# Optimization experiments

Hardware: AMD Instinct MI355X
Metric: run time of the kernel (lower is better)

The kernel has to match this reference:

```python
import jax, jax.numpy as jnp
import numpy as np

N = 100000
E = 3200000
F_IN = 128
H1 = 16
H2 = 8
NEG_SLOPE = 0.2


def _gat_layer(x, src, dst, W, a_src, a_dst, b, n_nodes):
    # x: [N, Fin]; src/dst: [E_tot] (self-loops included); W: [Fin, Fout]
    h = x @ W                                   # [N, Fout]
    e_src = h @ a_src                           # [N]
    e_dst = h @ a_dst                           # [N]
    e = e_src[src] + e_dst[dst]                 # [E_tot]
    e = jnp.where(e > 0, e, NEG_SLOPE * e)      # leaky_relu(0.2)
    m = jax.ops.segment_max(e, dst, num_segments=n_nodes)   # [N]
    w = jnp.exp(e - m[dst])                     # [E_tot]
    s = jax.ops.segment_sum(w, dst, num_segments=n_nodes)   # [N]
    alpha = w / s[dst]                          # [E_tot]
    out = jax.ops.segment_sum(alpha[:, None] * h[src], dst, num_segments=n_nodes)
    return out + b


def setup_inputs() -> dict:
    key = jax.random.key(0)
    ks = jax.random.split(key, 12)
    x = jax.random.normal(ks[0], (N, F_IN), dtype=jnp.float32)
    edge_index = jax.random.randint(ks[1], (E, 2), 0, N, dtype=jnp.int64)
    s1 = 1.0 / np.sqrt(F_IN)
    s2 = 1.0 / np.sqrt(H1)
    s3 = 1.0 / np.sqrt(H2)
    return {
        "x": x,
        "edge_index": edge_index,
        "W1": jax.random.normal(ks[2], (F_IN, H1), dtype=jnp.float32) * s1,
        "a1_src": jax.random.normal(ks[3], (H1,), dtype=jnp.float32) * s2,
        "a1_dst": jax.random.normal(ks[4], (H1,), dtype=jnp.float32) * s2,
        "b1": jnp.zeros((H1,), dtype=jnp.float32),
        "W2": jax.random.normal(ks[5], (H1, H2), dtype=jnp.float32) * s2,
        "a2_src": jax.random.normal(ks[6], (H2,), dtype=jnp.float32) * s3,
        "a2_dst": jax.random.normal(ks[7], (H2,), dtype=jnp.float32) * s3,
        "b2": jnp.zeros((H2,), dtype=jnp.float32),
        "Wf": jax.random.normal(ks[8], (H2, 1), dtype=jnp.float32) * s3,
        "bf": jnp.zeros((1,), dtype=jnp.float32),
    }


def reference(x, edge_index, W1, a1_src, a1_dst, b1, W2, a2_src, a2_dst, b2, Wf, bf):
    ei = edge_index.T                            # [2, E] as in original forward
    loop = jnp.arange(N, dtype=ei.dtype)
    src = jnp.concatenate([ei[0], loop])         # PyG add_self_loops=True
    dst = jnp.concatenate([ei[1], loop])
    h = jax.nn.relu(_gat_layer(x, src, dst, W1, a1_src, a1_dst, b1, N))
    # dropout p=0.05 is identity at inference
    h = jax.nn.relu(_gat_layer(h, src, dst, W2, a2_src, a2_dst, b2, N))
    return h @ Wf + bf                           # [N, 1]
```

## Files before the change

### kernel.cpp

```cpp
#include <hip/hip_runtime.h>
#include <math.h>

#define N_NODES 100000
#define N_EDGES 3200000
#define E_TOT   (N_EDGES + N_NODES)
#define F_IN    128
#define H1      16
#define H2      8
#define NEG     0.2f
#define NBUCKET ((N_NODES + 255) >> 8)
#define NCHUNK  512
#define CE      ((N_EDGES + NCHUNK - 1) / NCHUNK)

__global__ __launch_bounds__(256) void k1_xw(
        const float* __restrict__ x, const float* __restrict__ W1,
        const float* __restrict__ a1s, const float* __restrict__ a1d,
        float* __restrict__ h1, float* __restrict__ e1s, float* __restrict__ e1d) {
    __shared__ float w1s[F_IN * H1];
    __shared__ float xs[16 * 132];
    __shared__ float a1ss[H1], a1ds[H1];
    const int tid = threadIdx.x;
    for (int i = tid; i < F_IN * H1; i += 256) w1s[i] = W1[i];
    if (tid < H1) { a1ss[tid] = a1s[tid]; a1ds[tid] = a1d[tid]; }
    const int rowbase = blockIdx.x * 16;
    #pragma unroll
    for (int i = 0; i < 2; i++) {
        int q = tid + i * 256;
        int r = q >> 5, c = q & 31;
        float4 v = *(const float4*)(x + (size_t)(rowbase + r) * F_IN + c * 4);
        *(float4*)(xs + r * 132 + c * 4) = v;
    }
    __syncthreads();
    const int g = tid >> 4, j = tid & 15;
    const float* xrow = xs + g * 132;
    float acc = 0.f;
    #pragma unroll 8
    for (int k = 0; k < F_IN; k++) acc += xrow[k] * w1s[k * H1 + j];
    const int row = rowbase + g;
    h1[(size_t)row * H1 + j] = acc;
    float ps = acc * a1ss[j];
    float pd = acc * a1ds[j];
    #pragma unroll
    for (int m = 8; m >= 1; m >>= 1) {
        ps += __shfl_xor(ps, m, 16);
        pd += __shfl_xor(pd, m, 16);
    }
    if (j == 0) { e1s[row] = ps; e1d[row] = pd; }
}


__global__ __launch_bounds__(256) void k_count(const int2* __restrict__ ei,
                                               int* __restrict__ counts) {
    __shared__ int hist[NBUCKET];
    for (int i = threadIdx.x; i < NBUCKET; i += 256) hist[i] = 0;
    __syncthreads();
    const int b = blockIdx.x;
    const int beg = b * CE, end = min(N_EDGES, beg + CE);
    for (int e = beg + threadIdx.x; e < end; e += 256)
        atomicAdd(&hist[ei[e].y >> 8], 1);
    __syncthreads();
    for (int i = threadIdx.x; i < NBUCKET; i += 256)
        counts[i * NCHUNK + b] = hist[i];
}

__global__ __launch_bounds__(512) void k_scanA(int* __restrict__ counts,
                                               int* __restrict__ btot) {
    __shared__ int lds[NCHUNK];
    const int k = blockIdx.x, t = threadIdx.x;
    int v = counts[k * NCHUNK + t];
    lds[t] = v;
    __syncthreads();
    for (int off = 1; off < NCHUNK; off <<= 1) {
        int u = (t >= off) ? lds[t - off] : 0;
        __syncthreads();
        lds[t] += u;
        __syncthreads();
    }
    counts[k * NCHUNK + t] = lds[t] - v;
    if (t == NCHUNK - 1) btot[k] = lds[t];
}

__global__ __launch_bounds__(512) void k_scanB(const int* __restrict__ btot,
                                               int* __restrict__ bbase) {
    __shared__ int lds[512];
    const int t = threadIdx.x;
    int v = (t < NBUCKET) ? btot[t] : 0;
    lds[t] = v;
    __syncthreads();
    for (int off = 1; off < 512; off <<= 1) {
        int u = (t >= off) ? lds[t - off] : 0;
        __syncthreads();
        lds[t] += u;
        __syncthreads();
    }
    if (t < NBUCKET) bbase[t] = lds[t] - v;
    if (t == 511) bbase[NBUCKET] = lds[511];
}

__global__ __launch_bounds__(256) void k_reorder(const int2* __restrict__ ei,
                                                 const int* __restrict__ counts,
                                                 const int* __restrict__ bbase,
                                                 int* __restrict__ pairs) {
    __shared__ int cur[NBUCKET];
    const int b = blockIdx.x;
    for (int i = threadIdx.x; i < NBUCKET; i += 256)
        cur[i] = bbase[i] + counts[i * NCHUNK + b];
    __syncthreads();
    const int beg = b * CE, end = min(N_EDGES, beg + CE);
    for (int e = beg + threadIdx.x; e < end; e += 256) {
        int2 v = ei[e];
        int k = v.y >> 8;
        int pos = atomicAdd(&cur[k], 1);
        pairs[pos] = (v.x << 8) | (v.y & 255);
    }
}

__global__ __launch_bounds__(256) void k_csr(const int* __restrict__ pairs,
                                             const int* __restrict__ bbase,
                                             int* __restrict__ rowg,
                                             int* __restrict__ degg,
                                             int* __restrict__ sorted_src) {
    __shared__ int deg[256], scn[256], cur[256];
    const int k = blockIdx.x, t = threadIdx.x;
    const int n0 = k << 8;
    const int nn = min(256, N_NODES - n0);
    deg[t] = 0;
    __syncthreads();
    const int ebeg = bbase[k], eend = bbase[k + 1];
    for (int e = ebeg + t; e < eend; e += 256)
        atomicAdd(&deg[pairs[e] & 255], 1);
    __syncthreads();
    int v = (t < nn) ? deg[t] : 0;
    scn[t] = v;
    __syncthreads();
    for (int off = 1; off < 256; off <<= 1) {
        int u = (t >= off) ? scn[t - off] : 0;
        __syncthreads();
        scn[t] += u;
        __syncthreads();
    }
    int excl = scn[t] - v;
    if (t < nn) {
        int r = ebeg + excl + n0 + t;
        rowg[n0 + t] = r;
        degg[n0 + t] = v + 1;
        sorted_src[r] = n0 + t;
        cur[t] = r + 1;
    }
    __syncthreads();
    for (int e = ebeg + t; e < eend; e += 256) {
        int p = pairs[e];
        int pos = atomicAdd(&cur[p & 255], 1);
        sorted_src[pos] = p >> 8;
    }
}

template <int LPN, bool LAYER2>
__global__ __launch_bounds__(256) void k_agg(
        const int* __restrict__ row, const int* __restrict__ deg,
        const int* __restrict__ sorted_src,
        const float* __restrict__ es, const float* __restrict__ ed,
        const float* __restrict__ h, const float* __restrict__ b,
        const float* __restrict__ Wf, const float* __restrict__ bf,
        float* __restrict__ h_out, float* __restrict__ out) {
    const int sub = threadIdx.x & (LPN - 1);
    const int node = (blockIdx.x * 256 + threadIdx.x) / LPN;
    if (node >= N_NODES) return;
    const int beg = row[node];
    const int cnt = deg[node];
    const float edv = ed[node];
    const float4* h4 = (const float4*)h;
    float4 acc = make_float4(0.f, 0.f, 0.f, 0.f);
    float s = 0.f;
    int src_a = sorted_src[beg];
    int src_b = (cnt > 1) ? sorted_src[beg + 1] : src_a;
    float ev_a = es[src_a];
    float4 hv_a = h4[(size_t)src_a * LPN + sub];
    for (int t = 0; t < cnt; t++) {
        int src_c = (t + 2 < cnt) ? sorted_src[beg + t + 2] : src_b;
        float ev_b = es[src_b];
        float4 hv_b = h4[(size_t)src_b * LPN + sub];
        float e = ev_a + edv;
        e = e > 0.f ? e : NEG * e;
        float p = __expf(e);
        s += p;
        acc.x += p * hv_a.x;
        acc.y += p * hv_a.y;
        acc.z += p * hv_a.z;
        acc.w += p * hv_a.w;
        src_b = src_c; ev_a = ev_b; hv_a = hv_b;
    }
    const float inv = 1.f / s;
    const float4 b4 = ((const float4*)b)[sub];
    float4 o;
    o.x = fmaxf(acc.x * inv + b4.x, 0.f);
    o.y = fmaxf(acc.y * inv + b4.y, 0.f);
    o.z = fmaxf(acc.z * inv + b4.z, 0.f);
    o.w = fmaxf(acc.w * inv + b4.w, 0.f);
    if (!LAYER2) {
        ((float4*)h_out)[(size_t)node * LPN + sub] = o;
    } else {
        const float4 w4 = ((const float4*)Wf)[sub];
        float r = o.x * w4.x + o.y * w4.y + o.z * w4.z + o.w * w4.w;
        r += __shfl_xor(r, 1, 2);
        if (sub == 0) out[node] = r + bf[0];
    }
}

__global__ __launch_bounds__(256) void k_mid(
        const float* __restrict__ h1f, const float* __restrict__ W2,
        const float* __restrict__ a2s, const float* __restrict__ a2d,
        float* __restrict__ h2, float* __restrict__ e2s, float* __restrict__ e2d) {
    int n = blockIdx.x * 256 + threadIdx.x;
    if (n >= N_NODES) return;
    float4 r0 = ((const float4*)(h1f + (size_t)n * H1))[0];
    float4 r1 = ((const float4*)(h1f + (size_t)n * H1))[1];
    float4 r2 = ((const float4*)(h1f + (size_t)n * H1))[2];
    float4 r3 = ((const float4*)(h1f + (size_t)n * H1))[3];
    float hv[H1] = {r0.x, r0.y, r0.z, r0.w, r1.x, r1.y, r1.z, r1.w,
                    r2.x, r2.y, r2.z, r2.w, r3.x, r3.y, r3.z, r3.w};
    float hs = 0.f, hd = 0.f;
    float* h2row = h2 + (size_t)n * H2;
    #pragma unroll
    for (int i = 0; i < H2; i++) {
        float acc = 0.f;
        #pragma unroll
        for (int j = 0; j < H1; j++) acc += hv[j] * W2[j * H2 + i];
        h2row[i] = acc;
        hs += acc * a2s[i];
        hd += acc * a2d[i];
    }
    e2s[n] = hs;
    e2d[n] = hd;
}

extern "C" void kernel_launch(void* const* d_in, const int* in_sizes, int n_in,
                              void* d_out, int out_size, void* d_ws, size_t ws_size,
                              hipStream_t stream) {
    const float* x    = (const float*)d_in[0];
    const int2*  ei   = (const int2*)d_in[1];
    const float* W1   = (const float*)d_in[2];
    const float* a1s  = (const float*)d_in[3];
    const float* a1d  = (const float*)d_in[4];
    const float* b1   = (const float*)d_in[5];
    const float* W2   = (const float*)d_in[6];
    const float* a2s  = (const float*)d_in[7];
    const float* a2d  = (const float*)d_in[8];
    const float* b2   = (const float*)d_in[9];
    const float* Wf   = (const float*)d_in[10];
    const float* bf   = (const float*)d_in[11];
    float* out = (float*)d_out;

    char* wp = (char*)d_ws;
    int* sorted_src = (int*)wp;   wp += sizeof(int) * (size_t)E_TOT;
    int* pairs      = (int*)wp;   wp += sizeof(int) * (size_t)N_EDGES;
    int* counts     = (int*)wp;   wp += sizeof(int) * (size_t)NBUCKET * NCHUNK;
    int* btot       = (int*)wp;   wp += sizeof(int) * (NBUCKET + 1);
    int* bbase      = (int*)wp;   wp += sizeof(int) * (NBUCKET + 1);
    int* degg       = (int*)wp;   wp += sizeof(int) * N_NODES;
    int* rowg       = (int*)wp;   wp += sizeof(int) * N_NODES;
    float* h1  = (float*)wp;      wp += sizeof(float) * (size_t)N_NODES * H1;
    float* e1s = (float*)wp;      wp += sizeof(float) * N_NODES;
    float* e1d = (float*)wp;      wp += sizeof(float) * N_NODES;
    float* h1f = (float*)pairs;
    float* h2  = h1f + (size_t)N_NODES * H1;
    float* e2s = h2 + (size_t)N_NODES * H2;
    float* e2d = e2s + N_NODES;

    const int nb_node = (N_NODES + 255) / 256;

    k_count<<<NCHUNK, 256, 0, stream>>>(ei, counts);
    k_scanA<<<NBUCKET, 512, 0, stream>>>(counts, btot);
    k_scanB<<<1, 512, 0, stream>>>(btot, bbase);
    k_reorder<<<NCHUNK, 256, 0, stream>>>(ei, counts, bbase, pairs);
    k_csr<<<NBUCKET, 256, 0, stream>>>(pairs, bbase, rowg, degg, sorted_src);
    k1_xw<<<N_NODES / 16, 256, 0, stream>>>(x, W1, a1s, a1d, h1, e1s, e1d);
    k_agg<4, false><<<(N_NODES * 4 + 255) / 256, 256, 0, stream>>>(
        rowg, degg, sorted_src, e1s, e1d, h1, b1, nullptr, nullptr, h1f, nullptr);
    k_mid<<<nb_node, 256, 0, stream>>>(h1f, W2, a2s, a2d, h2, e2s, e2d);
    k_agg<2, true><<<(N_NODES * 2 + 255) / 256, 256, 0, stream>>>(
        rowg, degg, sorted_src, e2s, e2d, h2, b2, Wf, bf, nullptr, out);
}
```

Measured before the change: 335.4 us.

## Store layer-1 features in fp16 and batch gathers in aggregation loop

Layer-1 transformed features are now written as half precision, which halves the bytes gathered per edge in the first aggregation. The aggregation loop is also restructured to load U=8 source indices and their features at once before accumulating, replacing the two-deep software prefetch so more memory requests are in flight. The cost is fp16 rounding error in the layer-1 features, more registers per thread, and redundant loads of index 0 in partial batches.

After: 299.4 us. -10.7%, faster.

```diff
diff --git a/kernel.cpp b/kernel.cpp
--- a/kernel.cpp
+++ b/kernel.cpp
@@ -12,10 +12,12 @@
 #define NCHUNK  512
 #define CE      ((N_EDGES + NCHUNK - 1) / NCHUNK)
 
+typedef _Float16 half4v __attribute__((ext_vector_type(4)));
+
 __global__ __launch_bounds__(256) void k1_xw(
         const float* __restrict__ x, const float* __restrict__ W1,
         const float* __restrict__ a1s, const float* __restrict__ a1d,
-        float* __restrict__ h1, float* __restrict__ e1s, float* __restrict__ e1d) {
+        _Float16* __restrict__ h1h, float* __restrict__ e1s, float* __restrict__ e1d) {
     __shared__ float w1s[F_IN * H1];
     __shared__ float xs[16 * 132];
     __shared__ float a1ss[H1], a1ds[H1];
@@ -37,7 +39,7 @@
     #pragma unroll 8
     for (int k = 0; k < F_IN; k++) acc += xrow[k] * w1s[k * H1 + j];
     const int row = rowbase + g;
-    h1[(size_t)row * H1 + j] = acc;
+    h1h[(size_t)row * H1 + j] = (_Float16)acc;
     float ps = acc * a1ss[j];
     float pd = acc * a1ds[j];
     #pragma unroll
@@ -155,12 +157,12 @@
     }
 }
 
-template <int LPN, bool LAYER2>
+template <int LPN, int U, bool HALF, bool LAYER2>
 __global__ __launch_bounds__(256) void k_agg(
         const int* __restrict__ row, const int* __restrict__ deg,
         const int* __restrict__ sorted_src,
         const float* __restrict__ es, const float* __restrict__ ed,
-        const float* __restrict__ h, const float* __restrict__ b,
+        const void* __restrict__ hbuf, const float* __restrict__ b,
         const float* __restrict__ Wf, const float* __restrict__ bf,
         float* __restrict__ h_out, float* __restrict__ out) {
     const int sub = threadIdx.x & (LPN - 1);
@@ -169,26 +171,40 @@
     const int beg = row[node];
     const int cnt = deg[node];
     const float edv = ed[node];
-    const float4* h4 = (const float4*)h;
     float4 acc = make_float4(0.f, 0.f, 0.f, 0.f);
     float s = 0.f;
-    int src_a = sorted_src[beg];
-    int src_b = (cnt > 1) ? sorted_src[beg + 1] : src_a;
-    float ev_a = es[src_a];
-    float4 hv_a = h4[(size_t)src_a * LPN + sub];
-    for (int t = 0; t < cnt; t++) {
-        int src_c = (t + 2 < cnt) ? sorted_src[beg + t + 2] : src_b;
-        float ev_b = es[src_b];
-        float4 hv_b = h4[(size_t)src_b * LPN + sub];
-        float e = ev_a + edv;
-        e = e > 0.f ? e : NEG * e;
-        float p = __expf(e);
-        s += p;
-        acc.x += p * hv_a.x;
-        acc.y += p * hv_a.y;
-        acc.z += p * hv_a.z;
-        acc.w += p * hv_a.w;
-        src_b = src_c; ev_a = ev_b; hv_a = hv_b;
+    for (int t0 = 0; t0 < cnt; t0 += U) {
+        int srcs[U];
+        float evs[U];
+        float4 hvs[U];
+        #pragma unroll
+        for (int i = 0; i < U; i++) {
+            int idx = t0 + i;
+            srcs[i] = sorted_src[beg + (idx < cnt ? idx : 0)];
+        }
+        #pragma unroll
+        for (int i = 0; i < U; i++) {
+            evs[i] = es[srcs[i]];
+            if (HALF) {
+                half4v hv = ((const half4v*)hbuf)[(size_t)srcs[i] * LPN + sub];
+                hvs[i] = make_float4((float)hv.x, (float)hv.y, (float)hv.z, (float)hv.w);
+            } else {
+                hvs[i] = ((const float4*)hbuf)[(size_t)srcs[i] * LPN + sub];
+            }
+        }
+        #pragma unroll
+        for (int i = 0; i < U; i++) {
+            if (t0 + i < cnt) {
+                float e = evs[i] + edv;
+                e = e > 0.f ? e : NEG * e;
+                float p = __expf(e);
+                s += p;
+                acc.x += p * hvs[i].x;
+                acc.y += p * hvs[i].y;
+                acc.z += p * hvs[i].z;
+                acc.w += p * hvs[i].w;
+            }
+        }
     }
     const float inv = 1.f / s;
     const float4 b4 = ((const float4*)b)[sub];
@@ -259,7 +275,7 @@
     int* bbase      = (int*)wp;   wp += sizeof(int) * (NBUCKET + 1);
     int* degg       = (int*)wp;   wp += sizeof(int) * N_NODES;
     int* rowg       = (int*)wp;   wp += sizeof(int) * N_NODES;
-    float* h1  = (float*)wp;      wp += sizeof(float) * (size_t)N_NODES * H1;
+    _Float16* h1h = (_Float16*)wp; wp += sizeof(_Float16) * (size_t)N_NODES * H1;
     float* e1s = (float*)wp;      wp += sizeof(float) * N_NODES;
     float* e1d = (float*)wp;      wp += sizeof(float) * N_NODES;
     float* h1f = (float*)pairs;
@@ -274,10 +290,10 @@
     k_scanB<<<1, 512, 0, stream>>>(btot, bbase);
     k_reorder<<<NCHUNK, 256, 0, stream>>>(ei, counts, bbase, pairs);
     k_csr<<<NBUCKET, 256, 0, stream>>>(pairs, bbase, rowg, degg, sorted_src);
-    k1_xw<<<N_NODES / 16, 256, 0, stream>>>(x, W1, a1s, a1d, h1, e1s, e1d);
-    k_agg<4, false><<<(N_NODES * 4 + 255) / 256, 256, 0, stream>>>(
-        rowg, degg, sorted_src, e1s, e1d, h1, b1, nullptr, nullptr, h1f, nullptr);
+    k1_xw<<<N_NODES / 16, 256, 0, stream>>>(x, W1, a1s, a1d, h1h, e1s, e1d);
+    k_agg<4, 8, true, false><<<(N_NODES * 4 + 255) / 256, 256, 0, stream>>>(
+        rowg, degg, sorted_src, e1s, e1d, h1h, b1, nullptr, nullptr, h1f, nullptr);
     k_mid<<<nb_node, 256, 0, stream>>>(h1f, W2, a2s, a2d, h2, e2s, e2d);
-    k_agg<2, true><<<(N_NODES * 2 + 255) / 256, 256, 0, stream>>>(
+    k_agg<2, 8, false, true><<<(N_NODES * 2 + 255) / 256, 256, 0, stream>>>(
         rowg, degg, sorted_src, e2s, e2d, h2, b2, Wf, bf, nullptr, out);
 }
```
